# Performance work log

Measured on AMD Instinct MI355X. Metric: run time of the kernel, lower is better.

## Reference

```python
import jax, jax.numpy as jnp
import numpy as np

B, S, V, D = 64, 256, 50000, 300
NW, CL, CV, CD = 8192, 16, 500, 30
H, T, CH = 128, 17, 30


def setup_inputs() -> dict:
    key = jax.random.key(0)
    ks = jax.random.split(key, 32)
    f32 = jnp.float32
    def rn(k, shape, scale=0.1):
        return jax.random.normal(k, shape, dtype=f32) * scale
    inp = {}
    inp["char_emb"] = rn(ks[0], (CV, CD)).at[0].set(0.0)  # padding_idx=0
    inp["conv_w"] = rn(ks[1], (CH, CD, 3))  # OIH
    inp["conv_b"] = rn(ks[2], (CH,))
    inp["word_emb"] = rn(ks[3], (V, D))
    in0, in1 = D + CH, 2 * H
    inp["w_ih_l0"] = rn(ks[4], (2, 3 * H, in0))  # [dir, 3H, in]
    inp["w_hh_l0"] = rn(ks[5], (2, 3 * H, H))
    inp["b_ih_l0"] = rn(ks[6], (2, 3 * H))
    inp["b_hh_l0"] = rn(ks[7], (2, 3 * H))
    inp["w_ih_l1"] = rn(ks[8], (2, 3 * H, in1))
    inp["w_hh_l1"] = rn(ks[9], (2, 3 * H, H))
    inp["b_ih_l1"] = rn(ks[10], (2, 3 * H))
    inp["b_hh_l1"] = rn(ks[11], (2, 3 * H))
    inp["mlp_w1"] = rn(ks[12], (2 * H, H))
    inp["mlp_b1"] = rn(ks[13], (H,))
    inp["mlp_w2"] = rn(ks[14], (H, T))
    inp["mlp_b2"] = rn(ks[15], (T,))
    inp["crf_start"] = rn(ks[16], (T,))
    inp["crf_end"] = rn(ks[17], (T,))
    inp["crf_trans"] = rn(ks[18], (T, T))
    inp["batched_char_words"] = jax.random.randint(ks[19], (NW, CL), 0, CV)
    inp["batched_char_words_len"] = jax.random.randint(ks[20], (NW,), 1, CL + 1)
    inp["batched_char_word_index"] = jax.random.randint(ks[21], (B, S), 0, NW + 1)
    inp["batched_tokens"] = jax.random.randint(ks[22], (B, S), 0, V)
    inp["batched_tokens_len"] = jax.random.randint(ks[23], (B,), S // 2, S + 1)
    inp["target"] = jax.random.randint(ks[24], (B, S), 0, T)
    return inp


def _gru_dir(x, mask, w_ih, w_hh, b_ih, b_hh, reverse):
    # x: [B,S,I], mask: [B,S] bool. Masked (padded) steps carry hidden state
    # through unchanged, matching pack_padded_sequence semantics.
    xg = jnp.einsum('bsi,gi->sbg', x, w_ih) + b_ih  # [S,B,3H]
    m = mask.T  # [S,B]
    h0 = jnp.zeros((x.shape[0], w_hh.shape[1]), x.dtype)

    def step(h, inp):
        xt, mt = inp
        hg = h @ w_hh.T + b_hh
        xr, xz, xn = jnp.split(xt, 3, axis=-1)
        hr, hz, hn = jnp.split(hg, 3, axis=-1)
        r = jax.nn.sigmoid(xr + hr)
        z = jax.nn.sigmoid(xz + hz)
        n = jnp.tanh(xn + r * hn)
        hnew = (1.0 - z) * n + z * h
        h = jnp.where(mt[:, None], hnew, h)
        return h, h

    _, hs = jax.lax.scan(step, h0, (xg, m), reverse=reverse)
    return hs.transpose(1, 0, 2)  # [B,S,H]


def _bigru_layer(x, mask, w_ih, w_hh, b_ih, b_hh):
    fwd = _gru_dir(x, mask, w_ih[0], w_hh[0], b_ih[0], b_hh[0], False)
    bwd = _gru_dir(x, mask, w_ih[1], w_hh[1], b_ih[1], b_hh[1], True)
    return jnp.concatenate([fwd, bwd], axis=-1)


def _forward(char_emb, conv_w, conv_b, word_emb,
             w_ih_l0, w_hh_l0, b_ih_l0, b_hh_l0,
             w_ih_l1, w_hh_l1, b_ih_l1, b_hh_l1,
             mlp_w1, mlp_b1, mlp_w2, mlp_b2,
             crf_start, crf_end, crf_trans,
             batched_char_words, batched_char_word_index,
             batched_tokens, batched_tokens_len, target):
    # --- char CNN token encoder: conv1d(k=3, SAME) + relu + max-over-time ---
    ct = char_emb[batched_char_words]  # [NW,CL,CD]
    c = jax.lax.conv_general_dilated(ct.transpose(0, 2, 1), conv_w, (1,), 'SAME',
                                     dimension_numbers=('NCH', 'OIH', 'NCH'))
    c = jax.nn.relu(c + conv_b[None, :, None])
    tok_enc = jnp.max(c, axis=-1)  # [NW,CH]
    tok_enc = jnp.concatenate([jnp.zeros((1, tok_enc.shape[1]), tok_enc.dtype), tok_enc], axis=0)
    tok_idx = tok_enc[batched_char_word_index]  # [B,S,CH] (index 0 -> zeros)

    texts = jnp.concatenate([word_emb[batched_tokens], tok_idx], axis=-1)  # [B,S,D+CH]
    seq = batched_tokens.shape[1]
    mask = jnp.arange(seq)[None, :] < batched_tokens_len[:, None]  # [B,S]

    # --- 2-layer BiGRU ---
    h = _bigru_layer(texts, mask, w_ih_l0, w_hh_l0, b_ih_l0, b_hh_l0)
    h = _bigru_layer(h, mask, w_ih_l1, w_hh_l1, b_ih_l1, b_hh_l1)

    # --- MLP head -> emissions [B,S,17] ---
    h = jax.nn.relu(h @ mlp_w1 + mlp_b1)
    emissions = h @ mlp_w2 + mlp_b2

    # --- CRF negative log-likelihood, reduction='token_mean' ---
    maskf = mask.astype(emissions.dtype)
    emit_sc = jnp.take_along_axis(emissions, target[..., None], axis=-1)[..., 0]  # [B,S]
    trans_sc = crf_trans[target[:, :-1], target[:, 1:]]  # [B,S-1]
    score = crf_start[target[:, 0]] + emit_sc[:, 0]
    score = score + jnp.sum((trans_sc + emit_sc[:, 1:]) * maskf[:, 1:], axis=1)
    last_tags = jnp.take_along_axis(target, (batched_tokens_len - 1)[:, None], axis=1)[:, 0]
    score = score + crf_end[last_tags]

    alpha0 = crf_start[None, :] + emissions[:, 0]  # [B,T]
    em_rest = emissions[:, 1:].transpose(1, 0, 2)  # [S-1,B,T]
    m_rest = mask[:, 1:].T  # [S-1,B]

    def crf_step(alpha, inp):
        emit, mt = inp
        new = jax.nn.logsumexp(alpha[:, :, None] + crf_trans[None], axis=1) + emit
        return jnp.where(mt[:, None], new, alpha), None

    alpha, _ = jax.lax.scan(crf_step, alpha0, (em_rest, m_rest))
    log_z = jax.nn.logsumexp(alpha + crf_end[None, :], axis=1)
    llh = score - log_z
    return -(jnp.sum(llh) / jnp.sum(maskf))


def reference(char_emb, conv_w, conv_b, word_emb,
              w_ih_l0, w_hh_l0, b_ih_l0, b_hh_l0,
              w_ih_l1, w_hh_l1, b_ih_l1, b_hh_l1,
              mlp_w1, mlp_b1, mlp_w2, mlp_b2,
              crf_start, crf_end, crf_trans,
              batched_char_words, batched_char_words_len,
              batched_char_word_index, batched_tokens, batched_tokens_len, target):
    return _forward(char_emb, conv_w, conv_b, word_emb,
                    w_ih_l0, w_hh_l0, b_ih_l0, b_hh_l0,
                    w_ih_l1, w_hh_l1, b_ih_l1, b_hh_l1,
                    mlp_w1, mlp_b1, mlp_w2, mlp_b2,
                    crf_start, crf_end, crf_trans,
                    batched_char_words, batched_char_word_index,
                    batched_tokens, batched_tokens_len, target)
```

## Files before the change

### kernel.cpp

```cpp
#include <hip/hip_runtime.h>
#include <cstddef>

#define BATCH 64
#define SEQ   256
#define VOCAB 50000
#define DIM   300
#define NW    8192
#define CLEN  16
#define CDIM  30
#define CHC   30
#define HID   128
#define NT    17
#define IN0   (DIM + CHC)
#define IN0P  336
#define IN1   (2 * HID)
#define NPOS  (BATCH * SEQ)

constexpr size_t SZ_XG    = 2ull * BATCH * SEQ * 384;
constexpr size_t SZ_TEXTS = (size_t)NPOS * IN0P;
constexpr size_t SZ_H1    = (size_t)NPOS * 256;
constexpr size_t SZ_TOK   = 245792;
constexpr size_t SZ_EMIS  = (size_t)NPOS * NT;
constexpr size_t SZ_WPAD  = 768ull * IN0P;
constexpr size_t OFF_XG    = 0;
constexpr size_t OFF_TEXTS = OFF_XG + SZ_XG;
constexpr size_t OFF_H1    = OFF_TEXTS + SZ_TEXTS;
constexpr size_t OFF_TOK   = OFF_H1 + SZ_H1;
constexpr size_t OFF_EMIS  = OFF_TOK + SZ_TOK;
constexpr size_t OFF_WPAD  = OFF_EMIS + SZ_EMIS;
constexpr size_t OFF_LLH   = OFF_WPAD + SZ_WPAD;

__device__ __forceinline__ float sigm(float x) {
    return 1.f / (1.f + __expf(-x));
}
__device__ __forceinline__ float tanh_fast(float x) {
    x = fminf(fmaxf(x, -15.f), 15.f);
    float e = __expf(-2.f * x);
    return (1.f - e) / (1.f + e);
}
__device__ __forceinline__ float quad_sum(float x) {
    int y = __builtin_amdgcn_update_dpp(0, __float_as_int(x), 0xB1, 0xF, 0xF, false);
    x += __int_as_float(y);
    y = __builtin_amdgcn_update_dpp(0, __float_as_int(x), 0x4E, 0xF, 0xF, false);
    x += __int_as_float(y);
    return x;
}

__global__ __launch_bounds__(256) void char_conv_k(
    const float* __restrict__ char_emb,
    const float* __restrict__ conv_w,
    const float* __restrict__ conv_b,
    const int*   __restrict__ words,
    float* __restrict__ tok_enc)
{
    __shared__ __align__(16) float cs[8][CLEN][CDIM];
    __shared__ float wsm[CHC * CDIM * 3];
    __shared__ float bs[CHC];
    int n0 = blockIdx.x * 8;
    int tid = threadIdx.x;
    for (int e = tid; e < CHC * CDIM * 3; e += 256) wsm[e] = conv_w[e];
    if (tid < CHC) bs[tid] = conv_b[tid];
    for (int e = tid; e < 8 * CLEN * CDIM; e += 256) {
        int wi = e / (CLEN * CDIM);
        int rem = e - wi * (CLEN * CDIM);
        int l = rem / CDIM;
        int i = rem - l * CDIM;
        int ci = words[(n0 + wi) * CLEN + l];
        cs[wi][l][i] = char_emb[ci * CDIM + i];
    }
    __syncthreads();
    int wi = tid >> 5;
    int o = tid & 31;
    if (o < CHC) {
        float best = -1e30f;
        for (int l = 0; l < CLEN; l++) {
            float s = 0.f;
            #pragma unroll
            for (int k = 0; k < 3; k++) {
                int ll = l + k - 1;
                if (ll >= 0 && ll < CLEN) {
                    #pragma unroll
                    for (int i = 0; i < CDIM; i++)
                        s += cs[wi][ll][i] * wsm[(o * CDIM + i) * 3 + k];
                }
            }
            best = fmaxf(best, s);
        }
        tok_enc[(size_t)(n0 + wi + 1) * CDIM + o] = fmaxf(best + bs[o], 0.f);
    }
}

__global__ __launch_bounds__(128) void build_texts_k(
    const float* __restrict__ word_emb,
    const float* __restrict__ tok_enc,
    const int*   __restrict__ tokens,
    const int*   __restrict__ widx,
    float* __restrict__ texts)
{
    int p = blockIdx.x;
    int tok = tokens[p];
    int ci = widx[p];
    float* o = texts + (size_t)p * IN0P;
    const float* wr = word_emb + (size_t)tok * DIM;
    const float* tr = tok_enc + (size_t)ci * CDIM;
    for (int c = threadIdx.x; c < IN0P; c += 128)
        o[c] = (c < DIM) ? wr[c] : (c < IN0 ? tr[c - DIM] : 0.f);
}

__global__ __launch_bounds__(64) void pad_w_k(
    const float* __restrict__ w, float* __restrict__ wp)
{
    int r = blockIdx.x;
    for (int c = threadIdx.x; c < IN0P; c += 64)
        wp[(size_t)r * IN0P + c] = (c < IN0) ? w[(size_t)r * IN0 + c] : 0.f;
}

#define GBM 128
#define GBN 128
#define GBK 16
__global__ __launch_bounds__(256) void gemm_xg_k(
    const float* __restrict__ A,
    const float* __restrict__ W,
    const float* __restrict__ bias,
    float* __restrict__ out,
    int K)
{
    __shared__ __align__(16) float As[GBK][GBM];
    __shared__ __align__(16) float Ws[GBK][GBN];
    int tid = threadIdx.x;
    int m0 = blockIdx.x * GBM;
    int n0 = blockIdx.y * GBN;
    int lrow = tid >> 1;
    int lk = (tid & 1) * 8;
    int ty = tid >> 4;
    int tx = tid & 15;

    float acc[8][8];
    #pragma unroll
    for (int i = 0; i < 8; i++)
        #pragma unroll
        for (int j = 0; j < 8; j++) acc[i][j] = 0.f;

    for (int k0 = 0; k0 < K; k0 += GBK) {
        const float4* ap = (const float4*)(A + (size_t)(m0 + lrow) * K + k0 + lk);
        const float4* wp = (const float4*)(W + (size_t)(n0 + lrow) * K + k0 + lk);
        float4 va0 = ap[0], va1 = ap[1];
        float4 vw0 = wp[0], vw1 = wp[1];
        As[lk + 0][lrow] = va0.x; As[lk + 1][lrow] = va0.y;
        As[lk + 2][lrow] = va0.z; As[lk + 3][lrow] = va0.w;
        As[lk + 4][lrow] = va1.x; As[lk + 5][lrow] = va1.y;
        As[lk + 6][lrow] = va1.z; As[lk + 7][lrow] = va1.w;
        Ws[lk + 0][lrow] = vw0.x; Ws[lk + 1][lrow] = vw0.y;
        Ws[lk + 2][lrow] = vw0.z; Ws[lk + 3][lrow] = vw0.w;
        Ws[lk + 4][lrow] = vw1.x; Ws[lk + 5][lrow] = vw1.y;
        Ws[lk + 6][lrow] = vw1.z; Ws[lk + 7][lrow] = vw1.w;
        __syncthreads();
        #pragma unroll
        for (int k = 0; k < GBK; k++) {
            float4 a0 = *(const float4*)&As[k][ty * 8];
            float4 a1 = *(const float4*)&As[k][ty * 8 + 4];
            float4 b0 = *(const float4*)&Ws[k][tx * 8];
            float4 b1 = *(const float4*)&Ws[k][tx * 8 + 4];
            float av[8] = {a0.x, a0.y, a0.z, a0.w, a1.x, a1.y, a1.z, a1.w};
            float bv[8] = {b0.x, b0.y, b0.z, b0.w, b1.x, b1.y, b1.z, b1.w};
            #pragma unroll
            for (int i = 0; i < 8; i++)
                #pragma unroll
                for (int j = 0; j < 8; j++)
                    acc[i][j] += av[i] * bv[j];
        }
        __syncthreads();
    }
    int nb = n0 + tx * 8;
    int d = nb / 384;
    int g0 = nb - d * 384;
    float bvv[8];
    #pragma unroll
    for (int j = 0; j < 8; j++) bvv[j] = bias[nb + j];
    int mbase = m0 + ty * 8;
    #pragma unroll
    for (int i = 0; i < 8; i++) {
        int m = mbase + i;
        int b = m >> 8;
        int t = m & 255;
        float* op = out + (((size_t)(d * BATCH + b) * SEQ + t) * 384 + g0);
        #pragma unroll
        for (int j = 0; j < 8; j++) op[j] = acc[i][j] + bvv[j];
    }
}

__global__ __launch_bounds__(512, 2) void gru_rec_k(
    const float* __restrict__ xg,
    const float* __restrict__ w_hh,
    const float* __restrict__ b_hh,
    const int*   __restrict__ lens,
    float* __restrict__ out)
{
    int d = blockIdx.x & 1;
    int b = blockIdx.x >> 1;
    int i = threadIdx.x;
    int e = i >> 2;
    int c = i & 3;
    __shared__ __align__(16) float hS[2][HID];

    int rR = e, rZ = HID + e, rN = 2 * HID + e;
    const float* wbR = w_hh + ((size_t)d * 384 + rR) * HID + 32 * c;
    const float* wbZ = w_hh + ((size_t)d * 384 + rZ) * HID + 32 * c;
    const float* wbN = w_hh + ((size_t)d * 384 + rN) * HID + 32 * c;
    float4 wR[8], wZ[8], wN[8];
    #pragma unroll
    for (int q = 0; q < 8; q++) {
        int m = (q + c) & 7;
        wR[q] = *(const float4*)(wbR + 4 * m);
        wZ[q] = *(const float4*)(wbZ + 4 * m);
        wN[q] = *(const float4*)(wbN + 4 * m);
    }
    float bhR = b_hh[d * 384 + rR];
    float bhZ = b_hh[d * 384 + rZ];
    float bhN = b_hh[d * 384 + rN];
    int len = lens[b];

    if (i < HID) { hS[0][i] = 0.f; }
    float hold = 0.f;
    __syncthreads();

    const float* xgb = xg + ((size_t)(d * BATCH + b)) * SEQ * 384;
    float* outb = out + (size_t)b * SEQ * 256 + d * HID;

    int t0 = d ? (SEQ - 1) : 0;
    float xvR = xgb[(size_t)t0 * 384 + rR];
    float xvZ = xgb[(size_t)t0 * 384 + rZ];
    float xvN = xgb[(size_t)t0 * 384 + rN];
    int tPrev = 0;

    for (int s = 0; s < SEQ; s++) {
        int t = d ? (SEQ - 1 - s) : s;
        if (s && c == 0) outb[(size_t)tPrev * 256 + e] = hold;
        int sn = (s + 1 < SEQ) ? (s + 1) : s;
        int tn = d ? (SEQ - 1 - sn) : sn;
        float nxvR = xgb[(size_t)tn * 384 + rR];
        float nxvZ = xgb[(size_t)tn * 384 + rZ];
        float nxvN = xgb[(size_t)tn * 384 + rN];

        const float4* hb = (const float4*)hS[s & 1] + 8 * c;
        float sR = 0.f, sZ = 0.f, sN = 0.f;
        #pragma unroll
        for (int q = 0; q < 8; q++) {
            int m = (q + c) & 7;
            float4 hv = hb[m];
            sR += wR[q].x * hv.x + wR[q].y * hv.y + wR[q].z * hv.z + wR[q].w * hv.w;
            sZ += wZ[q].x * hv.x + wZ[q].y * hv.y + wZ[q].z * hv.z + wZ[q].w * hv.w;
            sN += wN[q].x * hv.x + wN[q].y * hv.y + wN[q].z * hv.z + wN[q].w * hv.w;
        }
        sR = quad_sum(sR);
        sZ = quad_sum(sZ);
        sN = quad_sum(sN);

        float r = sigm(xvR + sR + bhR);
        float z = sigm(xvZ + sZ + bhZ);
        float n = tanh_fast(xvN + r * (sN + bhN));
        float hnew = (1.f - z) * n + z * hold;
        hold = (t < len) ? hnew : hold;
        if (c == 0) hS[(s & 1) ^ 1][e] = hold;
        tPrev = t;
        xvR = nxvR; xvZ = nxvZ; xvN = nxvN;
        __syncthreads();
    }
    if (c == 0) outb[(size_t)tPrev * 256 + e] = hold;
}

__global__ __launch_bounds__(128) void mlp_emis_k(
    const float* __restrict__ h1,
    const float* __restrict__ w1,
    const float* __restrict__ b1,
    const float* __restrict__ w2,
    const float* __restrict__ b2,
    float* __restrict__ emis)
{
    __shared__ __align__(16) float hrow[8 * 256];
    __shared__ float hid[8][HID];
    int p0 = blockIdx.x * 8;
    int tid = threadIdx.x;
    for (int e = tid; e < 8 * 256; e += 128)
        hrow[e] = h1[(size_t)p0 * 256 + e];
    __syncthreads();
    float acc[8];
    float bb = b1[tid];
    #pragma unroll
    for (int i = 0; i < 8; i++) acc[i] = bb;
    for (int k = 0; k < 256; k++) {
        float wv = w1[k * HID + tid];
        #pragma unroll
        for (int i = 0; i < 8; i++) acc[i] += hrow[i * 256 + k] * wv;
    }
    #pragma unroll
    for (int i = 0; i < 8; i++) hid[i][tid] = fmaxf(acc[i], 0.f);
    __syncthreads();
    for (int idx = tid; idx < 8 * NT; idx += 128) {
        int pos = idx / NT;
        int tg = idx - pos * NT;
        float a = b2[tg];
        for (int k = 0; k < HID; k++) a += hid[pos][k] * w2[k * NT + tg];
        emis[(size_t)(p0 + pos) * NT + tg] = a;
    }
}

__global__ __launch_bounds__(64) void crf_k(
    const float* __restrict__ emis,
    const float* __restrict__ start,
    const float* __restrict__ endv,
    const float* __restrict__ trans,
    const int*   __restrict__ target,
    const int*   __restrict__ lens,
    float* __restrict__ llh)
{
    int b = blockIdx.x;
    int tid = threadIdx.x;
    __shared__ float tr[NT * NT];
    __shared__ float aSh[NT];
    __shared__ float scoreSh;
    for (int e = tid; e < NT * NT; e += 64) tr[e] = trans[e];
    __syncthreads();
    int len = lens[b];
    const int* tgt = target + b * SEQ;
    const float* eb = emis + (size_t)b * SEQ * NT;

    float part = 0.f;
    for (int t = 1 + tid; t < SEQ; t += 64) {
        if (t < len) {
            int tp = tgt[t - 1], tc = tgt[t];
            part += tr[tp * NT + tc] + eb[(size_t)t * NT + tc];
        }
    }
    #pragma unroll
    for (int off = 32; off > 0; off >>= 1)
        part += __shfl_down(part, off, 64);
    if (tid == 0) {
        int t0 = tgt[0];
        scoreSh = part + start[t0] + eb[t0] + endv[tgt[len - 1]];
    }

    float a = (tid < NT) ? (start[tid] + eb[tid]) : 0.f;
    for (int t = 1; t < SEQ; t++) {
        if (tid < NT) aSh[tid] = a;
        __syncthreads();
        if (t < len && tid < NT) {
            float m = -1e30f;
            #pragma unroll
            for (int i = 0; i < NT; i++)
                m = fmaxf(m, aSh[i] + tr[i * NT + tid]);
            float ssum = 0.f;
            #pragma unroll
            for (int i = 0; i < NT; i++)
                ssum += __expf(aSh[i] + tr[i * NT + tid] - m);
            a = m + __logf(ssum) + eb[(size_t)t * NT + tid];
        }
        __syncthreads();
    }
    float v = (tid < NT) ? (a + endv[tid]) : -1e30f;
    float m = v;
    #pragma unroll
    for (int off = 32; off > 0; off >>= 1)
        m = fmaxf(m, __shfl_down(m, off, 64));
    m = __shfl(m, 0, 64);
    float e = (tid < NT) ? __expf(v - m) : 0.f;
    #pragma unroll
    for (int off = 32; off > 0; off >>= 1)
        e += __shfl_down(e, off, 64);
    if (tid == 0) {
        float logz = m + __logf(e);
        llh[b] = scoreSh - logz;
    }
}

__global__ __launch_bounds__(64) void finalize_k(
    const float* __restrict__ llh,
    const int*   __restrict__ lens,
    float* __restrict__ out)
{
    int tid = threadIdx.x;
    float s = llh[tid];
    float lf = (float)lens[tid];
    #pragma unroll
    for (int off = 32; off > 0; off >>= 1) {
        s += __shfl_down(s, off, 64);
        lf += __shfl_down(lf, off, 64);
    }
    if (tid == 0) out[0] = -(s / lf);
}

extern "C" void kernel_launch(void* const* d_in, const int* in_sizes, int n_in,
                              void* d_out, int out_size, void* d_ws, size_t ws_size,
                              hipStream_t stream) {
    const float* char_emb = (const float*)d_in[0];
    const float* conv_w   = (const float*)d_in[1];
    const float* conv_b   = (const float*)d_in[2];
    const float* word_emb = (const float*)d_in[3];
    const float* w_ih_l0  = (const float*)d_in[4];
    const float* w_hh_l0  = (const float*)d_in[5];
    const float* b_ih_l0  = (const float*)d_in[6];
    const float* b_hh_l0  = (const float*)d_in[7];
    const float* w_ih_l1  = (const float*)d_in[8];
    const float* w_hh_l1  = (const float*)d_in[9];
    const float* b_ih_l1  = (const float*)d_in[10];
    const float* b_hh_l1  = (const float*)d_in[11];
    const float* mlp_w1   = (const float*)d_in[12];
    const float* mlp_b1   = (const float*)d_in[13];
    const float* mlp_w2   = (const float*)d_in[14];
    const float* mlp_b2   = (const float*)d_in[15];
    const float* crf_start= (const float*)d_in[16];
    const float* crf_end  = (const float*)d_in[17];
    const float* crf_trans= (const float*)d_in[18];
    const int* bcw   = (const int*)d_in[19];
    const int* bcwi  = (const int*)d_in[21];
    const int* btok  = (const int*)d_in[22];
    const int* blen  = (const int*)d_in[23];
    const int* target= (const int*)d_in[24];

    float* ws    = (float*)d_ws;
    float* xg    = ws + OFF_XG;
    float* texts = ws + OFF_TEXTS;
    float* h0    = texts;
    float* h1    = ws + OFF_H1;
    float* tok   = ws + OFF_TOK;
    float* emis  = ws + OFF_EMIS;
    float* wpad  = ws + OFF_WPAD;
    float* llh   = ws + OFF_LLH;

    hipMemsetAsync(tok, 0, CDIM * sizeof(float), stream);
    pad_w_k<<<768, 64, 0, stream>>>(w_ih_l0, wpad);
    char_conv_k<<<NW / 8, 256, 0, stream>>>(char_emb, conv_w, conv_b, bcw, tok);
    build_texts_k<<<NPOS, 128, 0, stream>>>(word_emb, tok, btok, bcwi, texts);
    gemm_xg_k<<<dim3(NPOS / GBM, 768 / GBN), 256, 0, stream>>>(texts, wpad, b_ih_l0, xg, IN0P);
    gru_rec_k<<<2 * BATCH, 512, 0, stream>>>(xg, w_hh_l0, b_hh_l0, blen, h0);
    gemm_xg_k<<<dim3(NPOS / GBM, 768 / GBN), 256, 0, stream>>>(h0, w_ih_l1, b_ih_l1, xg, IN1);
    gru_rec_k<<<2 * BATCH, 512, 0, stream>>>(xg, w_hh_l1, b_hh_l1, blen, h1);
    mlp_emis_k<<<NPOS / 8, 128, 0, stream>>>(h1, mlp_w1, mlp_b1, mlp_w2, mlp_b2, emis);
    crf_k<<<BATCH, 64, 0, stream>>>(emis, crf_start, crf_end, crf_trans, target, blen, llh);
    finalize_k<<<1, 64, 0, stream>>>(llh, blen, (float*)d_out);
}
```

Before: 879.5 us.

## Restructure char conv, GEMM tiling, and MLP loads for better reuse

```diff
diff --git a/kernel.cpp b/kernel.cpp
--- a/kernel.cpp
+++ b/kernel.cpp
@@ -53,37 +53,57 @@
     const int*   __restrict__ words,
     float* __restrict__ tok_enc)
 {
-    __shared__ __align__(16) float cs[8][CLEN][CDIM];
+    __shared__ __align__(16) float cs[8][CLEN][32];
     __shared__ float wsm[CHC * CDIM * 3];
     __shared__ float bs[CHC];
     int n0 = blockIdx.x * 8;
     int tid = threadIdx.x;
     for (int e = tid; e < CHC * CDIM * 3; e += 256) wsm[e] = conv_w[e];
     if (tid < CHC) bs[tid] = conv_b[tid];
-    for (int e = tid; e < 8 * CLEN * CDIM; e += 256) {
-        int wi = e / (CLEN * CDIM);
-        int rem = e - wi * (CLEN * CDIM);
-        int l = rem / CDIM;
-        int i = rem - l * CDIM;
-        int ci = words[(n0 + wi) * CLEN + l];
-        cs[wi][l][i] = char_emb[ci * CDIM + i];
+    for (int e = tid; e < 8 * CLEN * 32; e += 256) {
+        int wi = e >> 9;
+        int rem = e & 511;
+        int l = rem >> 5;
+        int ii = rem & 31;
+        float v = 0.f;
+        if (ii < CDIM) {
+            int ci = words[(n0 + wi) * CLEN + l];
+            v = char_emb[ci * CDIM + ii];
+        }
+        cs[wi][l][ii] = v;
     }
     __syncthreads();
     int wi = tid >> 5;
     int o = tid & 31;
     if (o < CHC) {
+        float wr[90];
+        #pragma unroll
+        for (int t = 0; t < 90; t++) wr[t] = wsm[o * 90 + t];
+        float P0[CLEN], P1[CLEN], P2[CLEN];
+        #pragma unroll
+        for (int l = 0; l < CLEN; l++) {
+            const float4* cr = (const float4*)cs[wi][l];
+            float s0 = 0.f, s1 = 0.f, s2 = 0.f;
+            #pragma unroll
+            for (int v4 = 0; v4 < 7; v4++) {
+                float4 cv = cr[v4];
+                int i0 = 4 * v4;
+                s0 += cv.x * wr[i0 * 3]     + cv.y * wr[(i0 + 1) * 3]     + cv.z * wr[(i0 + 2) * 3]     + cv.w * wr[(i0 + 3) * 3];
+                s1 += cv.x * wr[i0 * 3 + 1] + cv.y * wr[(i0 + 1) * 3 + 1] + cv.z * wr[(i0 + 2) * 3 + 1] + cv.w * wr[(i0 + 3) * 3 + 1];
+                s2 += cv.x * wr[i0 * 3 + 2] + cv.y * wr[(i0 + 1) * 3 + 2] + cv.z * wr[(i0 + 2) * 3 + 2] + cv.w * wr[(i0 + 3) * 3 + 2];
+            }
+            float4 cv7 = cr[7];
+            s0 += cv7.x * wr[84] + cv7.y * wr[87];
+            s1 += cv7.x * wr[85] + cv7.y * wr[88];
+            s2 += cv7.x * wr[86] + cv7.y * wr[89];
+            P0[l] = s0; P1[l] = s1; P2[l] = s2;
+        }
         float best = -1e30f;
-        for (int l = 0; l < CLEN; l++) {
-            float s = 0.f;
-            #pragma unroll
-            for (int k = 0; k < 3; k++) {
-                int ll = l + k - 1;
-                if (ll >= 0 && ll < CLEN) {
-                    #pragma unroll
-                    for (int i = 0; i < CDIM; i++)
-                        s += cs[wi][ll][i] * wsm[(o * CDIM + i) * 3 + k];
-                }
-            }
+        #pragma unroll
+        for (int lo = 0; lo < CLEN; lo++) {
+            float s = P1[lo];
+            if (lo > 0) s += P0[lo - 1];
+            if (lo < CLEN - 1) s += P2[lo + 1];
             best = fmaxf(best, s);
         }
         tok_enc[(size_t)(n0 + wi + 1) * CDIM + o] = fmaxf(best + bs[o], 0.f);
@@ -118,53 +138,60 @@
 #define GBM 128
 #define GBN 128
 #define GBK 16
-__global__ __launch_bounds__(256) void gemm_xg_k(
+#define GAMP 144
+#define GBNP 132
+__global__ __launch_bounds__(128, 2) void gemm_xg_k(
     const float* __restrict__ A,
     const float* __restrict__ W,
     const float* __restrict__ bias,
     float* __restrict__ out,
     int K)
 {
-    __shared__ __align__(16) float As[GBK][GBM];
-    __shared__ __align__(16) float Ws[GBK][GBN];
+    __shared__ __align__(16) float As[GBK][GAMP];
+    __shared__ __align__(16) float Ws[GBK][GBNP];
     int tid = threadIdx.x;
     int m0 = blockIdx.x * GBM;
     int n0 = blockIdx.y * GBN;
-    int lrow = tid >> 1;
-    int lk = (tid & 1) * 8;
+    int acol = tid + 4 * (tid >> 5);
+    int wcol = tid + 4 * ((tid >> 5) & 1);
     int ty = tid >> 4;
     int tx = tid & 15;
-
-    float acc[8][8];
-    #pragma unroll
-    for (int i = 0; i < 8; i++)
+    int abase = ty * 16 + 4 * (ty >> 1);
+    int bbase = tx * 8 + 4 * ((tx >> 2) & 1);
+
+    float acc[16][8];
+    #pragma unroll
+    for (int i = 0; i < 16; i++)
         #pragma unroll
         for (int j = 0; j < 8; j++) acc[i][j] = 0.f;
 
     for (int k0 = 0; k0 < K; k0 += GBK) {
-        const float4* ap = (const float4*)(A + (size_t)(m0 + lrow) * K + k0 + lk);
-        const float4* wp = (const float4*)(W + (size_t)(n0 + lrow) * K + k0 + lk);
-        float4 va0 = ap[0], va1 = ap[1];
-        float4 vw0 = wp[0], vw1 = wp[1];
-        As[lk + 0][lrow] = va0.x; As[lk + 1][lrow] = va0.y;
-        As[lk + 2][lrow] = va0.z; As[lk + 3][lrow] = va0.w;
-        As[lk + 4][lrow] = va1.x; As[lk + 5][lrow] = va1.y;
-        As[lk + 6][lrow] = va1.z; As[lk + 7][lrow] = va1.w;
-        Ws[lk + 0][lrow] = vw0.x; Ws[lk + 1][lrow] = vw0.y;
-        Ws[lk + 2][lrow] = vw0.z; Ws[lk + 3][lrow] = vw0.w;
-        Ws[lk + 4][lrow] = vw1.x; Ws[lk + 5][lrow] = vw1.y;
-        Ws[lk + 6][lrow] = vw1.z; Ws[lk + 7][lrow] = vw1.w;
+        const float4* ap = (const float4*)(A + (size_t)(m0 + tid) * K + k0);
+        const float4* wp = (const float4*)(W + (size_t)(n0 + tid) * K + k0);
+        float4 va0 = ap[0], va1 = ap[1], va2 = ap[2], va3 = ap[3];
+        float4 vw0 = wp[0], vw1 = wp[1], vw2 = wp[2], vw3 = wp[3];
+        As[0][acol] = va0.x;  As[1][acol] = va0.y;  As[2][acol] = va0.z;  As[3][acol] = va0.w;
+        As[4][acol] = va1.x;  As[5][acol] = va1.y;  As[6][acol] = va1.z;  As[7][acol] = va1.w;
+        As[8][acol] = va2.x;  As[9][acol] = va2.y;  As[10][acol] = va2.z; As[11][acol] = va2.w;
+        As[12][acol] = va3.x; As[13][acol] = va3.y; As[14][acol] = va3.z; As[15][acol] = va3.w;
+        Ws[0][wcol] = vw0.x;  Ws[1][wcol] = vw0.y;  Ws[2][wcol] = vw0.z;  Ws[3][wcol] = vw0.w;
+        Ws[4][wcol] = vw1.x;  Ws[5][wcol] = vw1.y;  Ws[6][wcol] = vw1.z;  Ws[7][wcol] = vw1.w;
+        Ws[8][wcol] = vw2.x;  Ws[9][wcol] = vw2.y;  Ws[10][wcol] = vw2.z; Ws[11][wcol] = vw2.w;
+        Ws[12][wcol] = vw3.x; Ws[13][wcol] = vw3.y; Ws[14][wcol] = vw3.z; Ws[15][wcol] = vw3.w;
         __syncthreads();
         #pragma unroll
         for (int k = 0; k < GBK; k++) {
-            float4 a0 = *(const float4*)&As[k][ty * 8];
-            float4 a1 = *(const float4*)&As[k][ty * 8 + 4];
-            float4 b0 = *(const float4*)&Ws[k][tx * 8];
-            float4 b1 = *(const float4*)&Ws[k][tx * 8 + 4];
-            float av[8] = {a0.x, a0.y, a0.z, a0.w, a1.x, a1.y, a1.z, a1.w};
-            float bv[8] = {b0.x, b0.y, b0.z, b0.w, b1.x, b1.y, b1.z, b1.w};
+            float4 a0 = *(const float4*)&As[k][abase];
+            float4 a1 = *(const float4*)&As[k][abase + 4];
+            float4 a2 = *(const float4*)&As[k][abase + 8];
+            float4 a3 = *(const float4*)&As[k][abase + 12];
+            float4 b0 = *(const float4*)&Ws[k][bbase];
+            float4 b1 = *(const float4*)&Ws[k][bbase + 4];
+            float av[16] = {a0.x, a0.y, a0.z, a0.w, a1.x, a1.y, a1.z, a1.w,
+                            a2.x, a2.y, a2.z, a2.w, a3.x, a3.y, a3.z, a3.w};
+            float bv[8]  = {b0.x, b0.y, b0.z, b0.w, b1.x, b1.y, b1.z, b1.w};
             #pragma unroll
-            for (int i = 0; i < 8; i++)
+            for (int i = 0; i < 16; i++)
                 #pragma unroll
                 for (int j = 0; j < 8; j++)
                     acc[i][j] += av[i] * bv[j];
@@ -177,9 +204,9 @@
     float bvv[8];
     #pragma unroll
     for (int j = 0; j < 8; j++) bvv[j] = bias[nb + j];
-    int mbase = m0 + ty * 8;
-    #pragma unroll
-    for (int i = 0; i < 8; i++) {
+    int mbase = m0 + ty * 16;
+    #pragma unroll
+    for (int i = 0; i < 16; i++) {
         int m = mbase + i;
         int b = m >> 8;
         int t = m & 255;
@@ -220,7 +247,7 @@
     float bhN = b_hh[d * 384 + rN];
     int len = lens[b];
 
-    if (i < HID) { hS[0][i] = 0.f; }
+    if (i < HID) hS[0][i] = 0.f;
     float hold = 0.f;
     __syncthreads();
 
@@ -281,17 +308,29 @@
     __shared__ float hid[8][HID];
     int p0 = blockIdx.x * 8;
     int tid = threadIdx.x;
-    for (int e = tid; e < 8 * 256; e += 128)
-        hrow[e] = h1[(size_t)p0 * 256 + e];
+    {
+        const float4* hv = (const float4*)(h1 + (size_t)p0 * 256);
+        float4* hw = (float4*)hrow;
+        #pragma unroll
+        for (int e = tid; e < 512; e += 128) hw[e] = hv[e];
+    }
     __syncthreads();
     float acc[8];
     float bb = b1[tid];
     #pragma unroll
     for (int i = 0; i < 8; i++) acc[i] = bb;
-    for (int k = 0; k < 256; k++) {
-        float wv = w1[k * HID + tid];
-        #pragma unroll
-        for (int i = 0; i < 8; i++) acc[i] += hrow[i * 256 + k] * wv;
+    const float4* hrow4 = (const float4*)hrow;
+    for (int k4 = 0; k4 < 64; k4++) {
+        int k = 4 * k4;
+        float w0 = w1[k * HID + tid];
+        float w1v = w1[(k + 1) * HID + tid];
+        float w2v = w1[(k + 2) * HID + tid];
+        float w3v = w1[(k + 3) * HID + tid];
+        #pragma unroll
+        for (int i = 0; i < 8; i++) {
+            float4 h4 = hrow4[i * 64 + k4];
+            acc[i] += h4.x * w0 + h4.y * w1v + h4.z * w2v + h4.w * w3v;
+        }
     }
     #pragma unroll
     for (int i = 0; i < 8; i++) hid[i][tid] = fmaxf(acc[i], 0.f);
@@ -431,9 +470,9 @@
     pad_w_k<<<768, 64, 0, stream>>>(w_ih_l0, wpad);
     char_conv_k<<<NW / 8, 256, 0, stream>>>(char_emb, conv_w, conv_b, bcw, tok);
     build_texts_k<<<NPOS, 128, 0, stream>>>(word_emb, tok, btok, bcwi, texts);
-    gemm_xg_k<<<dim3(NPOS / GBM, 768 / GBN), 256, 0, stream>>>(texts, wpad, b_ih_l0, xg, IN0P);
+    gemm_xg_k<<<dim3(NPOS / GBM, 768 / GBN), 128, 0, stream>>>(texts, wpad, b_ih_l0, xg, IN0P);
     gru_rec_k<<<2 * BATCH, 512, 0, stream>>>(xg, w_hh_l0, b_hh_l0, blen, h0);
-    gemm_xg_k<<<dim3(NPOS / GBM, 768 / GBN), 256, 0, stream>>>(h0, w_ih_l1, b_ih_l1, xg, IN1);
+    gemm_xg_k<<<dim3(NPOS / GBM, 768 / GBN), 128, 0, stream>>>(h0, w_ih_l1, b_ih_l1, xg, IN1);
     gru_rec_k<<<2 * BATCH, 512, 0, stream>>>(xg, w_hh_l1, b_hh_l1, blen, h1);
     mlp_emis_k<<<NPOS / 8, 128, 0, stream>>>(h1, mlp_w1, mlp_b1, mlp_w2, mlp_b2, emis);
     crf_k<<<BATCH, 64, 0, stream>>>(emis, crf_start, crf_end, crf_trans, target, blen, llh);
```

After: 904.5 us. 2.8% more time.
